# Kernel optimization log

Hardware: AMD Instinct MI355X
Metric: run time of the kernel (lower is better)

## Reference

```python
import jax, jax.numpy as jnp
import numpy as np

B = 262144          # batch of independent thermostat states
L = 64              # hidden width l
SIG_RANGE = 10.0    # SigmoidLinear range
T_ON = 66.0
T_OFF = 78.0
N_STEPS = 40        # While(target_idx=[0], test=40.0), step starts at 0


def setup_inputs() -> dict:
    key = jax.random.key(0)
    k0, k1, k2, k3, k4 = jax.random.split(key, 5)
    step = jnp.zeros((B,), jnp.float32)
    isOn = jnp.round(jax.random.uniform(k0, (B,), jnp.float32))
    temp = jax.random.uniform(k1, (B,), jnp.float32, minval=55.0, maxval=85.0)
    aux = jax.random.uniform(k2, (B,), jnp.float32)
    x_init = jnp.stack([step, isOn, temp, aux], axis=-1)  # [B, 4]
    W1 = jax.random.normal(k3, (2, L), jnp.float32) * 0.5
    b1 = jnp.zeros((L,), jnp.float32)
    W2 = jax.random.normal(k4, (L, 1), jnp.float32) * 0.5
    b2 = jnp.zeros((1,), jnp.float32)
    return {"x_init": x_init, "W1": W1, "b1": b1, "W2": W2, "b2": b2}


def _plant_nn(temp, aux, W1, b1, W2, b2):
    # LinearReLU: Linear(2->L) -> ReLU -> Linear(L->1) -> SigmoidLinear(sig_range)
    inp = jnp.stack([temp, aux], axis=-1)            # [B, 2]
    h = jax.nn.relu(inp @ W1 + b1)                   # [B, L]
    s = jax.nn.sigmoid(h @ W2 + b2)[..., 0]          # [B]
    return s * SIG_RANGE - SIG_RANGE / 2.0           # map to [-range/2, range/2]


def reference(x_init, W1, b1, W2, b2):
    def body(state, _):
        step = state[:, 0]
        isOn = state[:, 1]
        temp = state[:, 2]
        aux = state[:, 3]
        active = step < N_STEPS  # data-dependent while guard (masked scan)
        plant = _plant_nn(temp, aux, W1, b1, W2, b2)
        dtemp = plant * 10.0
        off = isOn <= 0.5
        # cooling branch (isOn <= 0.5): temp += plant*10; if temp <= tOn: isOn = 1
        # heating branch: temp += plant*10 + 5;        if temp >  tOff: isOn = 0
        temp_new = jnp.where(off, temp + dtemp, temp + dtemp + 5.0)
        isOn_new = jnp.where(
            off,
            jnp.where(temp_new <= T_ON, 1.0, isOn),
            jnp.where(temp_new <= T_OFF, isOn, 0.0),
        )
        temp2 = jnp.where(active, temp_new, temp)
        isOn2 = jnp.where(active, isOn_new, isOn)
        step2 = jnp.where(active, step + 1.0, step)
        new_state = jnp.stack([step2, isOn2, temp2, aux], axis=-1)
        return new_state, temp2  # Trajectory(target_idx=[2]) records temperature

    final_state, traj = jax.lax.scan(body, x_init, None, length=N_STEPS)
    return traj  # [N_STEPS, B] temperature trajectory
```

## Files before the change

kernel.cpp:

```cpp
#include <hip/hip_runtime.h>
#include <math.h>


#define LHID 64
#define NSTEPS 40

__global__ __launch_bounds__(256, 2) void thermostat_kernel(
    const float* __restrict__ x_init,
    const float* __restrict__ W1,
    const float* __restrict__ b1,
    const float* __restrict__ W2,
    const float* __restrict__ b2,
    float* __restrict__ out,
    int B)
{
    __shared__ __align__(16) float lds_a[LHID];
    __shared__ __align__(16) float lds_w2[LHID];

    int tid = threadIdx.x;
    if (tid < LHID) {
        lds_a[tid]  = W1[tid];
        lds_w2[tid] = W2[tid];
    }
    __syncthreads();

    int b = blockIdx.x * blockDim.x + tid;
    if (b >= B) return;

    float4 st = reinterpret_cast<const float4*>(x_init)[b];
    float step0 = st.x;
    float isOn  = st.y;
    float temp  = st.z;
    float aux   = st.w;
    float bias2 = b2[0];

    int n_active = (int)ceilf(fminf(fmaxf((float)NSTEPS - step0, 0.0f), (float)NSTEPS));

    float c[LHID];
#pragma unroll
    for (int j = 0; j < LHID; j += 4) {
        float4 vr1 = *reinterpret_cast<const float4*>(&W1[LHID + j]);
        float4 vb  = *reinterpret_cast<const float4*>(&b1[j]);
        c[j+0] = fmaf(aux, vr1.x, vb.x);
        c[j+1] = fmaf(aux, vr1.y, vb.y);
        c[j+2] = fmaf(aux, vr1.z, vb.z);
        c[j+3] = fmaf(aux, vr1.w, vb.w);
    }
#pragma unroll
    for (int j = 0; j < LHID; ++j) {
        asm volatile("" : "+v"(c[j]));
    }

    float* po = out + b;

#pragma unroll 1
    for (int t = 0; t < NSTEPS; ++t) {
        float acc = 0.0f;
#pragma unroll
        for (int j = 0; j < LHID; j += 4) {
            float4 av = *reinterpret_cast<const float4*>(&lds_a[j]);
            float4 wv = *reinterpret_cast<const float4*>(&lds_w2[j]);
            float h0 = fmaxf(fmaf(temp, av.x, c[j+0]), 0.0f); acc = fmaf(h0, wv.x, acc);
            float h1 = fmaxf(fmaf(temp, av.y, c[j+1]), 0.0f); acc = fmaf(h1, wv.y, acc);
            float h2 = fmaxf(fmaf(temp, av.z, c[j+2]), 0.0f); acc = fmaf(h2, wv.z, acc);
            float h3 = fmaxf(fmaf(temp, av.w, c[j+3]), 0.0f); acc = fmaf(h3, wv.w, acc);
        }
        float x = __fadd_rn(acc, bias2);

        float e = expf(-fabsf(x));
        float num = (x >= 0.0f) ? 1.0f : e;
        float s = num / (1.0f + e);

        float plant = __fsub_rn(__fmul_rn(s, 10.0f), 5.0f);
        float dtemp = __fmul_rn(plant, 10.0f);

        float tn_off = __fadd_rn(temp, dtemp);
        float tn_on  = __fadd_rn(tn_off, 5.0f);

        bool off = (isOn <= 0.5f);
        float temp_new = off ? tn_off : tn_on;
        float isOn_new;
        if (off) isOn_new = (temp_new <= 66.0f) ? 1.0f : isOn;
        else     isOn_new = (temp_new <= 78.0f) ? isOn : 0.0f;

        if (t < n_active) {
            temp = temp_new;
            isOn = isOn_new;
        }

        *po = temp;
        po += B;
    }
}

extern "C" void kernel_launch(void* const* d_in, const int* in_sizes, int n_in,
                              void* d_out, int out_size, void* d_ws, size_t ws_size,
                              hipStream_t stream) {
    const float* x_init = (const float*)d_in[0];
    const float* W1     = (const float*)d_in[1];
    const float* b1     = (const float*)d_in[2];
    const float* W2     = (const float*)d_in[3];
    const float* b2     = (const float*)d_in[4];
    float* out = (float*)d_out;

    int B = in_sizes[0] / 4;
    int threads = 256;
    int blocks = (B + threads - 1) / threads;
    thermostat_kernel<<<blocks, threads, 0, stream>>>(x_init, W1, b1, W2, b2, out, B);
}
```

Measured before the change: 55.51 us.

## Hand-schedule hidden-layer loop in inline asm with pinned registers and interleaved weights

Replaces the compiler-generated inner MLP loop with hand-written GCN assembly. The precomputed per-neuron biases are pinned to fixed VGPRs, W1 and W2 are interleaved in a single LDS array, and double-buffered ds_read_b128 loads are overlapped with the FMA/max chain using explicit lgkmcnt waits. Launch bounds drop to 1 block per CU minimum, which gives the allocator more registers. The aim is to hide LDS latency and avoid compiler spills or rematerialisation. Risks include fragile hardcoded register numbers and changed occupancy, and the n_active rounding switches from ceil to truncation.

```diff
diff --git a/kernel.cpp b/kernel.cpp
--- a/kernel.cpp
+++ b/kernel.cpp
@@ -5,7 +5,49 @@
 #define LHID 64
 #define NSTEPS 40
 
-__global__ __launch_bounds__(256, 2) void thermostat_kernel(
+typedef __attribute__((ext_vector_type(4))) float f32x4;
+
+#define PINQ(N0, N1, N2, N3, QV, S0, S1, S2, S3)                               \
+    asm volatile("v_mov_b32 v" #N0 ", %1\n\t"                                  \
+                 "v_mov_b32 v" #N1 ", %2\n\t"                                  \
+                 "v_mov_b32 v" #N2 ", %3\n\t"                                  \
+                 "v_mov_b32 v" #N3 ", %4"                                      \
+                 : "=&{v[" #N0 ":" #N3 "]}"(QV)                                \
+                 : "v"(S0), "v"(S1), "v"(S2), "v"(S3))
+
+#define QUAD(A0, W0, CE, A1, W1, CO)                                           \
+    "v_fma_f32 v136, %1, " A0 ", " CE "\n\t"                                   \
+    "v_fma_f32 v137, %1, " A1 ", " CO "\n\t"                                   \
+    "v_max_f32 v136, 0, v136\n\t"                                              \
+    "v_max_f32 v137, 0, v137\n\t"                                              \
+    "v_fmac_f32 %0, v136, " W0 "\n\t"                                          \
+    "v_fmac_f32 %0, v137, " W1 "\n\t"
+
+#define GA(C0,C1,C2,C3,C4,C5,C6,C7)                                            \
+    QUAD("v104","v105",C0,"v106","v107",C1)                                    \
+    QUAD("v108","v109",C2,"v110","v111",C3)                                    \
+    QUAD("v112","v113",C4,"v114","v115",C5)                                    \
+    QUAD("v116","v117",C6,"v118","v119",C7)
+
+#define GB(C0,C1,C2,C3,C4,C5,C6,C7)                                            \
+    QUAD("v120","v121",C0,"v122","v123",C1)                                    \
+    QUAD("v124","v125",C2,"v126","v127",C3)                                    \
+    QUAD("v128","v129",C4,"v130","v131",C5)                                    \
+    QUAD("v132","v133",C6,"v134","v135",C7)
+
+#define LA(O0,O1,O2,O3)                                                        \
+    "ds_read_b128 v[104:107], %2 offset:" O0 "\n\t"                            \
+    "ds_read_b128 v[108:111], %2 offset:" O1 "\n\t"                            \
+    "ds_read_b128 v[112:115], %2 offset:" O2 "\n\t"                            \
+    "ds_read_b128 v[116:119], %2 offset:" O3 "\n\t"
+
+#define LB(O0,O1,O2,O3)                                                        \
+    "ds_read_b128 v[120:123], %2 offset:" O0 "\n\t"                            \
+    "ds_read_b128 v[124:127], %2 offset:" O1 "\n\t"                            \
+    "ds_read_b128 v[128:131], %2 offset:" O2 "\n\t"                            \
+    "ds_read_b128 v[132:135], %2 offset:" O3 "\n\t"
+
+__global__ __launch_bounds__(256, 1) void thermostat_kernel(
     const float* __restrict__ x_init,
     const float* __restrict__ W1,
     const float* __restrict__ b1,
@@ -14,13 +56,11 @@
     float* __restrict__ out,
     int B)
 {
-    __shared__ __align__(16) float lds_a[LHID];
-    __shared__ __align__(16) float lds_w2[LHID];
+    __shared__ __align__(16) float lds_w[2 * LHID];
 
     int tid = threadIdx.x;
-    if (tid < LHID) {
-        lds_a[tid]  = W1[tid];
-        lds_w2[tid] = W2[tid];
+    if (tid < 2 * LHID) {
+        lds_w[tid] = (tid & 1) ? W2[tid >> 1] : W1[tid >> 1];
     }
     __syncthreads();
 
@@ -34,7 +74,7 @@
     float aux   = st.w;
     float bias2 = b2[0];
 
-    int n_active = (int)ceilf(fminf(fmaxf((float)NSTEPS - step0, 0.0f), (float)NSTEPS));
+    int n_active = (int)fminf(fmaxf((float)NSTEPS - step0, 0.0f), (float)NSTEPS);
 
     float c[LHID];
 #pragma unroll
@@ -46,25 +86,73 @@
         c[j+2] = fmaf(aux, vr1.z, vb.z);
         c[j+3] = fmaf(aux, vr1.w, vb.w);
     }
-#pragma unroll
-    for (int j = 0; j < LHID; ++j) {
-        asm volatile("" : "+v"(c[j]));
-    }
 
+    f32x4 cq0, cq1, cq2, cq3, cq4, cq5, cq6, cq7;
+    f32x4 cq8, cq9, cq10, cq11, cq12, cq13, cq14, cq15;
+    PINQ(40,41,42,43,    cq0,  c[0],  c[1],  c[2],  c[3]);
+    PINQ(44,45,46,47,    cq1,  c[4],  c[5],  c[6],  c[7]);
+    PINQ(48,49,50,51,    cq2,  c[8],  c[9],  c[10], c[11]);
+    PINQ(52,53,54,55,    cq3,  c[12], c[13], c[14], c[15]);
+    PINQ(56,57,58,59,    cq4,  c[16], c[17], c[18], c[19]);
+    PINQ(60,61,62,63,    cq5,  c[20], c[21], c[22], c[23]);
+    PINQ(64,65,66,67,    cq6,  c[24], c[25], c[26], c[27]);
+    PINQ(68,69,70,71,    cq7,  c[28], c[29], c[30], c[31]);
+    PINQ(72,73,74,75,    cq8,  c[32], c[33], c[34], c[35]);
+    PINQ(76,77,78,79,    cq9,  c[36], c[37], c[38], c[39]);
+    PINQ(80,81,82,83,    cq10, c[40], c[41], c[42], c[43]);
+    PINQ(84,85,86,87,    cq11, c[44], c[45], c[46], c[47]);
+    PINQ(88,89,90,91,    cq12, c[48], c[49], c[50], c[51]);
+    PINQ(92,93,94,95,    cq13, c[52], c[53], c[54], c[55]);
+    PINQ(96,97,98,99,    cq14, c[56], c[57], c[58], c[59]);
+    PINQ(100,101,102,103,cq15, c[60], c[61], c[62], c[63]);
+
+    unsigned lbase = (unsigned)(uintptr_t)(void*)lds_w;
     float* po = out + b;
 
 #pragma unroll 1
     for (int t = 0; t < NSTEPS; ++t) {
         float acc = 0.0f;
-#pragma unroll
-        for (int j = 0; j < LHID; j += 4) {
-            float4 av = *reinterpret_cast<const float4*>(&lds_a[j]);
-            float4 wv = *reinterpret_cast<const float4*>(&lds_w2[j]);
-            float h0 = fmaxf(fmaf(temp, av.x, c[j+0]), 0.0f); acc = fmaf(h0, wv.x, acc);
-            float h1 = fmaxf(fmaf(temp, av.y, c[j+1]), 0.0f); acc = fmaf(h1, wv.y, acc);
-            float h2 = fmaxf(fmaf(temp, av.z, c[j+2]), 0.0f); acc = fmaf(h2, wv.z, acc);
-            float h3 = fmaxf(fmaf(temp, av.w, c[j+3]), 0.0f); acc = fmaf(h3, wv.w, acc);
-        }
+        asm volatile(
+            LA("0","16","32","48")
+            LB("64","80","96","112")
+            "s_waitcnt lgkmcnt(4)\n\t"
+            GA("v40","v41","v42","v43","v44","v45","v46","v47")
+            LA("128","144","160","176")
+            "s_waitcnt lgkmcnt(4)\n\t"
+            GB("v48","v49","v50","v51","v52","v53","v54","v55")
+            LB("192","208","224","240")
+            "s_waitcnt lgkmcnt(4)\n\t"
+            GA("v56","v57","v58","v59","v60","v61","v62","v63")
+            LA("256","272","288","304")
+            "s_waitcnt lgkmcnt(4)\n\t"
+            GB("v64","v65","v66","v67","v68","v69","v70","v71")
+            LB("320","336","352","368")
+            "s_waitcnt lgkmcnt(4)\n\t"
+            GA("v72","v73","v74","v75","v76","v77","v78","v79")
+            LA("384","400","416","432")
+            "s_waitcnt lgkmcnt(4)\n\t"
+            GB("v80","v81","v82","v83","v84","v85","v86","v87")
+            LB("448","464","480","496")
+            "s_waitcnt lgkmcnt(4)\n\t"
+            GA("v88","v89","v90","v91","v92","v93","v94","v95")
+            "s_waitcnt lgkmcnt(0)\n\t"
+            GB("v96","v97","v98","v99","v100","v101","v102","v103")
+            : "+v"(acc)
+            : "v"(temp), "v"(lbase),
+              "{v[40:43]}"(cq0),   "{v[44:47]}"(cq1),
+              "{v[48:51]}"(cq2),   "{v[52:55]}"(cq3),
+              "{v[56:59]}"(cq4),   "{v[60:63]}"(cq5),
+              "{v[64:67]}"(cq6),   "{v[68:71]}"(cq7),
+              "{v[72:75]}"(cq8),   "{v[76:79]}"(cq9),
+              "{v[80:83]}"(cq10),  "{v[84:87]}"(cq11),
+              "{v[88:91]}"(cq12),  "{v[92:95]}"(cq13),
+              "{v[96:99]}"(cq14),  "{v[100:103]}"(cq15)
+            : "v104","v105","v106","v107","v108","v109","v110","v111",
+              "v112","v113","v114","v115","v116","v117","v118","v119",
+              "v120","v121","v122","v123","v124","v125","v126","v127",
+              "v128","v129","v130","v131","v132","v133","v134","v135",
+              "v136","v137");
+
         float x = __fadd_rn(acc, bias2);
 
         float e = expf(-fabsf(x));
```

Result: slower. 63.55 us (+14.5%).
